# Kernel optimization log

Hardware: AMD Instinct MI355X
Metric: run time of the kernel (lower is better)

## Reference

```python
import jax, jax.numpy as jnp
import numpy as np

B, S, EMBED, HEADS = 2, 2048, 1024, 16
HEAD = EMBED // HEADS


def setup_inputs() -> dict:
    key = jax.random.key(0)
    ks = jax.random.split(key, 8)
    inp = {
        "values": jax.random.normal(ks[0], (B, S, EMBED), jnp.float32),
        "keys": jax.random.normal(ks[1], (B, S, EMBED), jnp.float32),
        "queries": jax.random.normal(ks[2], (B, S, EMBED), jnp.float32),
        # causal mask, broadcast over batch and heads; masked_fill where mask==0
        "mask": jnp.tril(jnp.ones((S, S), jnp.bool_))[None, None, :, :],
        # torch nn.Linear weights: y = x @ W.T (+ b)
        "Wv": jax.random.normal(ks[3], (HEAD, HEAD), jnp.float32) / np.sqrt(HEAD),
        "Wk": jax.random.normal(ks[4], (HEAD, HEAD), jnp.float32) / np.sqrt(HEAD),
        "Wq": jax.random.normal(ks[5], (HEAD, HEAD), jnp.float32) / np.sqrt(HEAD),
        "Wo": jax.random.normal(ks[6], (EMBED, EMBED), jnp.float32) / np.sqrt(EMBED),
        "bo": jax.random.normal(ks[7], (EMBED,), jnp.float32) * 0.01,
    }
    return inp


def reference(values, keys, queries, mask, Wv, Wk, Wq, Wo, bo):
    N, Lq = queries.shape[0], queries.shape[1]
    Lk = keys.shape[1]
    # split heads: [B, L, H, D]
    v = values.reshape(N, -1, HEADS, HEAD) @ Wv.T
    k = keys.reshape(N, Lk, HEADS, HEAD) @ Wk.T
    q = queries.reshape(N, Lq, HEADS, HEAD) @ Wq.T
    # scores [B, H, Lq, Lk]
    energy = jnp.einsum('bqhd,bkhd->bhqk', q, k)
    energy = jnp.where(mask, energy, jnp.float32(-1e20))
    attn = jax.nn.softmax(energy / np.sqrt(HEAD), axis=-1)
    out = jnp.einsum('bhqk,bkhd->bqhd', attn, v).reshape(N, Lq, EMBED)
    return out @ Wo.T + bo
```

## Files before the change

kernel.cpp:

```cpp
#include <hip/hip_runtime.h>
#include <hip/hip_bf16.h>
#include <math.h>

constexpr int Bc = 2;
constexpr int Sc = 2048;
constexpr int E  = 1024;
constexpr int Hn = 16;
constexpr int Dh = 64;

typedef short bf16x8 __attribute__((ext_vector_type(8)));
typedef float f32x4  __attribute__((ext_vector_type(4)));

#define MFMA16(a, b, c) __builtin_amdgcn_mfma_f32_16x16x32_bf16((a), (b), (c), 0, 0, 0)

constexpr float QSCALE = 0.125f * 1.4426950408889634f;
constexpr float FIXED_M2 = 18.0f;

__device__ inline bf16x8 load8(const __hip_bfloat16* p) {
    return *reinterpret_cast<const bf16x8*>(p);
}

__device__ inline unsigned short f2b(float x) {
    __hip_bfloat16 h = __float2bfloat16(x);
    unsigned short u;
    __builtin_memcpy(&u, &h, 2);
    return u;
}

__device__ inline ushort4 pack4(float a, float b, float c, float d) {
    __hip_bfloat162 lo = __float22bfloat162_rn(make_float2(a, b));
    __hip_bfloat162 hi = __float22bfloat162_rn(make_float2(c, d));
    ushort4 u;
    __builtin_memcpy(&u.x, &lo, 4);
    __builtin_memcpy(&u.z, &hi, 4);
    return u;
}

__device__ inline bf16x8 cvt8(const float* p) {
    float4 a = *reinterpret_cast<const float4*>(p);
    float4 b = *reinterpret_cast<const float4*>(p + 4);
    ushort4 lo = pack4(a.x, a.y, a.z, a.w);
    ushort4 hi = pack4(b.x, b.y, b.z, b.w);
    bf16x8 r;
    __builtin_memcpy(&r, &lo, 8);
    __builtin_memcpy(reinterpret_cast<char*>(&r) + 8, &hi, 8);
    return r;
}

__device__ inline float fast_exp2(float x) {
#if __has_builtin(__builtin_amdgcn_exp2f)
    return __builtin_amdgcn_exp2f(x);
#else
    return exp2f(x);
#endif
}


__global__ __launch_bounds__(256) void cvt_w(
    const float* __restrict__ Wo, const float* __restrict__ Wq,
    const float* __restrict__ Wk, const float* __restrict__ Wv,
    __hip_bfloat16* __restrict__ Wf, __hip_bfloat16* __restrict__ Wf3) {
    const int i = blockIdx.x * 256 + threadIdx.x;
    if (i < 131072) {
        const int l16 = i & 15, quad = (i >> 4) & 3;
        const int kk = (i >> 6) & 31, ct = i >> 11;
        bf16x8 v = cvt8(Wo + (size_t)(ct * 16 + l16) * E + kk * 32 + quad * 8);
        *reinterpret_cast<bf16x8*>(Wf + (size_t)i * 8) = v;
    } else {
        const int idx = i - 131072;
        const int m = idx >> 9, r = idx & 511;
        const int lane = r & 63, nh = r >> 6;
        const int nt = nh >> 1, half = nh & 1;
        const int quad = lane >> 4, l16 = lane & 15;
        const float* Wm = (m == 0) ? Wq : (m == 1) ? Wk : Wv;
        bf16x8 v = cvt8(Wm + (nt * 16 + l16) * 64 + half * 32 + quad * 8);
        *reinterpret_cast<bf16x8*>(Wf3 + (size_t)idx * 8) = v;
    }
}

__global__ __launch_bounds__(256) void qkv_proj(
    const float* __restrict__ vals,
    const float* __restrict__ keys,
    const float* __restrict__ quer,
    const __hip_bfloat16* __restrict__ Wf3,
    __hip_bfloat16* __restrict__ Qf,
    __hip_bfloat16* __restrict__ Kf,
    __hip_bfloat16* __restrict__ Vf)
{
    __shared__ __align__(16) __hip_bfloat16 X[3][64 * 72];

    const int bid = blockIdx.x;
    const int st  = bid & 31;
    const int h   = (bid >> 5) & 15;
    const int b   = bid >> 9;
    const int sbase = st * 64;
    const int tid = threadIdx.x;

    const float* srcs[3] = { quer, keys, vals };
#pragma unroll
    for (int m = 0; m < 3; ++m) {
        for (int i = tid; i < 512; i += 256) {
            const int r = i >> 3, c = i & 7;
            bf16x8 v = cvt8(srcs[m] + (size_t)(b * Sc + sbase + r) * E + h * 64 + c * 8);
            *reinterpret_cast<bf16x8*>(&X[m][r * 72 + c * 8]) = v;
        }
    }
    __syncthreads();

    const int lane = tid & 63, w = tid >> 6;
    const int quad = lane >> 4, l16 = lane & 15;
    const int bh = b * Hn + h;
    const size_t bhoff = (size_t)bh * 131072;

#pragma unroll
    for (int m = 0; m < 2; ++m) {
        bf16x8 xb0 = load8(&X[m][(w * 16 + l16) * 72 + quad * 8]);
        bf16x8 xb1 = load8(&X[m][(w * 16 + l16) * 72 + quad * 8 + 32]);
#pragma unroll
        for (int ntd = 0; ntd < 4; ++ntd) {
            bf16x8 wa0 = load8(Wf3 + ((size_t)(m * 8 + ntd * 2 + 0) * 64 + lane) * 8);
            bf16x8 wa1 = load8(Wf3 + ((size_t)(m * 8 + ntd * 2 + 1) * 64 + lane) * 8);
            f32x4 acc = (f32x4){0.f, 0.f, 0.f, 0.f};
            acc = MFMA16(wa0, xb0, acc);
            acc = MFMA16(wa1, xb1, acc);
            const int half   = ntd >> 1;
            const int quad_f = (ntd & 1) * 2 + (quad >> 1);
            const int j0     = (quad & 1) * 4;
            if (m == 0) {
                const int t = st * 4 + w;
                *reinterpret_cast<ushort4*>(
                    Qf + bhoff + ((size_t)(t * 2 + half) * 64 + quad_f * 16 + l16) * 8 + j0) =
                    pack4(acc[0] * QSCALE, acc[1] * QSCALE, acc[2] * QSCALE, acc[3] * QSCALE);
            } else {
                *reinterpret_cast<ushort4*>(
                    Kf + bhoff + (((size_t)(st * 4 + w) * 2 + half) * 64 + quad_f * 16 + l16) * 8 + j0) =
                    pack4(acc[0], acc[1], acc[2], acc[3]);
            }
        }
    }

    {
        bf16x8 xa0 = load8(&X[2][(w * 16 + l16) * 72 + quad * 8]);
        bf16x8 xa1 = load8(&X[2][(w * 16 + l16) * 72 + quad * 8 + 32]);
        const int half   = w >> 1;
        const int quad_f = (w & 1) * 2 + (quad >> 1);
        const int j0     = (quad & 1) * 4;
#pragma unroll
        for (int nt = 0; nt < 4; ++nt) {
            bf16x8 wb0 = load8(Wf3 + ((size_t)(16 + nt * 2 + 0) * 64 + lane) * 8);
            bf16x8 wb1 = load8(Wf3 + ((size_t)(16 + nt * 2 + 1) * 64 + lane) * 8);
            f32x4 acc = (f32x4){0.f, 0.f, 0.f, 0.f};
            acc = MFMA16(xa0, wb0, acc);
            acc = MFMA16(xa1, wb1, acc);
            *reinterpret_cast<ushort4*>(
                Vf + bhoff + (((size_t)(st * 4 + nt) * 2 + half) * 64 + quad_f * 16 + l16) * 8 + j0) =
                pack4(acc[0], acc[1], acc[2], acc[3]);
        }
    }
}

__global__ __launch_bounds__(256) void flash_attn(
    const __hip_bfloat16* __restrict__ Qf,
    const __hip_bfloat16* __restrict__ Kf,
    const __hip_bfloat16* __restrict__ Vf,
    __hip_bfloat16* __restrict__ Af)
{
    __shared__ __align__(16) __hip_bfloat16 P[4][16 * 72];
    __shared__ __align__(16) float OB[4][16 * 68];
    __shared__ float LB[4][16];

    const int bid = blockIdx.x;
    const int bh = bid & 31;
    const int ip = bid >> 5;
    const int h  = bh & 15;
    const int b  = bh >> 4;
    const int tid = threadIdx.x, lane = tid & 63, w = tid >> 6;
    const int quad = lane >> 4, l16 = lane & 15;
    const int p  = w >> 1;
    const int hf = w & 1;
    const int j  = ip * 2 + p;

    const __hip_bfloat16* Qp = Qf + (size_t)bh * 131072;
    const __hip_bfloat16* Kp = Kf + (size_t)bh * 131072;
    const __hip_bfloat16* Vp = Vf + (size_t)bh * 131072;

    bf16x8 onesf;
#pragma unroll
    for (int q = 0; q < 8; ++q) onesf[q] = (short)0x3F80;

#pragma unroll
    for (int side = 0; side < 2; ++side) {
        const int t  = side ? j : (127 - j);
        const int nk = (t >> 2) + 1;
        const int r0 = t * 16;

        const bf16x8 qf0 = load8(Qp + ((size_t)(t * 2 + 0) * 64 + lane) * 8);
        const bf16x8 qf1 = load8(Qp + ((size_t)(t * 2 + 1) * 64 + lane) * 8);

        f32x4 oa[4];
#pragma unroll
        for (int nt = 0; nt < 4; ++nt) oa[nt] = (f32x4){0.f, 0.f, 0.f, 0.f};
        f32x4 lsacc = (f32x4){0.f, 0.f, 0.f, 0.f};

        if (hf < nk) {
            bf16x8 ka[4], kb[4];
#pragma unroll
            for (int nt = 0; nt < 4; ++nt) {
                const size_t o = (((size_t)hf * 4 + nt) * 2) * 64 * 8;
                ka[nt] = load8(Kp + o + lane * 8);
                kb[nt] = load8(Kp + o + 512 + lane * 8);
            }
            for (int kt = hf; kt < nk; kt += 2) {
                bf16x8 va[4], vb[4];
#pragma unroll
                for (int nt = 0; nt < 4; ++nt) {
                    const size_t o = (((size_t)kt * 4 + nt) * 2) * 64 * 8;
                    va[nt] = load8(Vp + o + lane * 8);
                    vb[nt] = load8(Vp + o + 512 + lane * 8);
                }
                const int nkt = (kt + 2 < nk) ? kt + 2 : kt;
                bf16x8 na[4], nb[4];
#pragma unroll
                for (int nt = 0; nt < 4; ++nt) {
                    const size_t o = (((size_t)nkt * 4 + nt) * 2) * 64 * 8;
                    na[nt] = load8(Kp + o + lane * 8);
                    nb[nt] = load8(Kp + o + 512 + lane * 8);
                }
                const int kbase = kt * 64;
                f32x4 sc[4];
#pragma unroll
                for (int ntk = 0; ntk < 4; ++ntk) {
                    f32x4 z = (f32x4){0.f, 0.f, 0.f, 0.f};
                    z = MFMA16(ka[ntk], qf0, z);
                    z = MFMA16(kb[ntk], qf1, z);
                    sc[ntk] = z;
                }
                if (kt == nk - 1) {
                    const int qrow = r0 + l16;
#pragma unroll
                    for (int ntk = 0; ntk < 4; ++ntk) {
#pragma unroll
                        for (int r = 0; r < 4; ++r)
                            if (kbase + ntk * 16 + quad * 4 + r > qrow)
                                sc[ntk][r] = -1e30f;
                    }
                }
#pragma unroll
                for (int ntk = 0; ntk < 4; ++ntk) {
                    const float p0 = fast_exp2(sc[ntk][0] - FIXED_M2);
                    const float p1 = fast_exp2(sc[ntk][1] - FIXED_M2);
                    const float p2 = fast_exp2(sc[ntk][2] - FIXED_M2);
                    const float p3 = fast_exp2(sc[ntk][3] - FIXED_M2);
                    *reinterpret_cast<ushort4*>(
                        &P[w][l16 * 72 + ntk * 16 + quad * 4]) = pack4(p0, p1, p2, p3);
                }
                bf16x8 pf0 = load8(&P[w][l16 * 72 + quad * 8]);
                bf16x8 pf1 = load8(&P[w][l16 * 72 + quad * 8 + 32]);
#pragma unroll
                for (int nt = 0; nt < 4; ++nt) {
                    oa[nt] = MFMA16(va[nt], pf0, oa[nt]);
                    oa[nt] = MFMA16(vb[nt], pf1, oa[nt]);
                }
                lsacc = MFMA16(onesf, pf0, lsacc);
                lsacc = MFMA16(onesf, pf1, lsacc);
#pragma unroll
                for (int nt = 0; nt < 4; ++nt) { ka[nt] = na[nt]; kb[nt] = nb[nt]; }
            }
        }
        const float ls = lsacc[0];

        const int slot = p * 2 + side;
        if (hf == 1) {
#pragma unroll
            for (int nt = 0; nt < 4; ++nt)
                *reinterpret_cast<float4*>(&OB[slot][l16 * 68 + nt * 16 + quad * 4]) =
                    (float4){ oa[nt][0], oa[nt][1], oa[nt][2], oa[nt][3] };
            if (quad == 0) LB[slot][l16] = ls;
        }
        __syncthreads();
        if (hf == 0) {
            const float inv = 1.0f / (ls + LB[slot][l16]);
            const int rt = b * 128 + t;
#pragma unroll
            for (int nt = 0; nt < 4; ++nt) {
                float4 ob = *reinterpret_cast<float4*>(&OB[slot][l16 * 68 + nt * 16 + quad * 4]);
                const int kk     = h * 2 + (nt >> 1);
                const int quad_f = (nt & 1) * 2 + (quad >> 1);
                const int j0     = (quad & 1) * 4;
                *reinterpret_cast<ushort4*>(
                    Af + (((size_t)rt * 32 + kk) * 64 + quad_f * 16 + l16) * 8 + j0) =
                    pack4((oa[nt][0] + ob.x) * inv, (oa[nt][1] + ob.y) * inv,
                          (oa[nt][2] + ob.z) * inv, (oa[nt][3] + ob.w) * inv);
            }
        }
    }
}

__global__ __launch_bounds__(256) void out_proj(
    const __hip_bfloat16* __restrict__ Af,
    const __hip_bfloat16* __restrict__ Wf,
    const float* __restrict__ bo,
    float* __restrict__ out)
{
    const int bid = blockIdx.x;
    const int cb = bid & 15;
    const int rb = bid >> 4;
    const int tid = threadIdx.x, lane = tid & 63, w = tid >> 6;
    const int quad = lane >> 4, l16 = lane & 15;
    const int rt0 = rb * 8 + w;
    const int cbase = cb * 64;

    const __hip_bfloat16* pa0 = Af + ((size_t)rt0 * 32) * 512 + lane * 8;
    const __hip_bfloat16* pa1 = pa0 + 4 * 32 * 512;
    const __hip_bfloat16* pw  = Wf + ((size_t)cb * 4 * 32) * 512 + lane * 8;

    f32x4 acc[2][4];
#pragma unroll
    for (int u = 0; u < 2; ++u)
#pragma unroll
        for (int nt = 0; nt < 4; ++nt) acc[u][nt] = (f32x4){0.f, 0.f, 0.f, 0.f};

    bf16x8 af0[2], af1[2], bf[4][2];
#pragma unroll
    for (int s = 0; s < 2; ++s) {
        const size_t ko = (size_t)s * 512;
        af0[s] = load8(pa0 + ko);
        af1[s] = load8(pa1 + ko);
#pragma unroll
        for (int nt = 0; nt < 4; ++nt) bf[nt][s] = load8(pw + (size_t)nt * 32 * 512 + ko);
    }

    for (int kk = 0; kk < 32; kk += 2) {
#pragma unroll
        for (int s = 0; s < 2; ++s) {
            const int kn = kk + 2 + s;
            const size_t ko = (size_t)((kn < 32) ? kn : kk + s) * 512;
            bf16x8 naf0 = load8(pa0 + ko), naf1 = load8(pa1 + ko);
            bf16x8 nbf[4];
#pragma unroll
            for (int nt = 0; nt < 4; ++nt) nbf[nt] = load8(pw + (size_t)nt * 32 * 512 + ko);
#pragma unroll
            for (int nt = 0; nt < 4; ++nt) {
                acc[0][nt] = MFMA16(af0[s], bf[nt][s], acc[0][nt]);
                acc[1][nt] = MFMA16(af1[s], bf[nt][s], acc[1][nt]);
            }
            af0[s] = naf0; af1[s] = naf1;
#pragma unroll
            for (int nt = 0; nt < 4; ++nt) bf[nt][s] = nbf[nt];
        }
    }
#pragma unroll
    for (int nt = 0; nt < 4; ++nt) {
        const float bv = bo[cbase + nt * 16 + l16];
#pragma unroll
        for (int u = 0; u < 2; ++u)
#pragma unroll
            for (int r = 0; r < 4; ++r) {
                const int row = (rt0 + u * 4) * 16 + quad * 4 + r;
                out[(size_t)row * E + cbase + nt * 16 + l16] = acc[u][nt][r] + bv;
            }
    }
}

extern "C" void kernel_launch(void* const* d_in, const int* in_sizes, int n_in,
                              void* d_out, int out_size, void* d_ws, size_t ws_size,
                              hipStream_t stream) {
    const float* vals = (const float*)d_in[0];
    const float* keys = (const float*)d_in[1];
    const float* quer = (const float*)d_in[2];
    const float* Wv = (const float*)d_in[4];
    const float* Wk = (const float*)d_in[5];
    const float* Wq = (const float*)d_in[6];
    const float* Wo = (const float*)d_in[7];
    const float* bo = (const float*)d_in[8];
    float* out = (float*)d_out;

    __hip_bfloat16* ws = (__hip_bfloat16*)d_ws;
    constexpr size_t NTOK = (size_t)Bc * Hn * Sc * Dh;
    __hip_bfloat16* Qw  = ws;
    __hip_bfloat16* Kw  = ws + NTOK;
    __hip_bfloat16* Vw  = ws + 2 * NTOK;
    __hip_bfloat16* Aw  = ws + 3 * NTOK;
    __hip_bfloat16* Wof = ws + 4 * NTOK;
    __hip_bfloat16* Wf3 = Wof + (size_t)E * E;

    hipLaunchKernelGGL(cvt_w, dim3(518), dim3(256), 0, stream, Wo, Wq, Wk, Wv, Wof, Wf3);
    hipLaunchKernelGGL(qkv_proj, dim3(Bc * Hn * (Sc / 64)), dim3(256), 0, stream,
                       vals, keys, quer, Wf3, Qw, Kw, Vw);
    hipLaunchKernelGGL(flash_attn, dim3(32 * 32), dim3(256), 0, stream,
                       Qw, Kw, Vw, Aw);
    hipLaunchKernelGGL(out_proj, dim3(32 * 16), dim3(256), 0, stream,
                       Aw, Wof, bo, out);
}
```

Measured before the change: 176.6 us.

## Process two adjacent query tiles per wave sharing K/V loads, longest blocks first

Flash attention blocks now use two waves that each handle a pair of adjacent 16-row query tiles, so every K and V fragment loaded is reused for two query tiles. The old front/back pairing of query tiles for load balance is replaced by a grid of 128-thread blocks ordered so the heaviest (longest causal) blocks launch first. The fixed softmax offset is folded into the MFMA accumulator init, and K prefetching across iterations is dropped. This cuts global K/V traffic per query row but raises register pressure and removes software prefetch.

```diff
diff --git a/kernel.cpp b/kernel.cpp
--- a/kernel.cpp
+++ b/kernel.cpp
@@ -159,26 +159,25 @@
     }
 }
 
-__global__ __launch_bounds__(256) void flash_attn(
+__global__ __launch_bounds__(128, 4) void flash_attn(
     const __hip_bfloat16* __restrict__ Qf,
     const __hip_bfloat16* __restrict__ Kf,
     const __hip_bfloat16* __restrict__ Vf,
     __hip_bfloat16* __restrict__ Af)
 {
-    __shared__ __align__(16) __hip_bfloat16 P[4][16 * 72];
-    __shared__ __align__(16) float OB[4][16 * 68];
-    __shared__ float LB[4][16];
+    __shared__ __align__(16) __hip_bfloat16 P[2][2][16 * 72];
+    __shared__ __align__(16) float OB[2][16 * 68];
+    __shared__ float LB[2][16];
 
     const int bid = blockIdx.x;
     const int bh = bid & 31;
-    const int ip = bid >> 5;
+    const int u  = 63 - (bid >> 5);
     const int h  = bh & 15;
     const int b  = bh >> 4;
-    const int tid = threadIdx.x, lane = tid & 63, w = tid >> 6;
+    const int tid = threadIdx.x, lane = tid & 63, hf = tid >> 6;
     const int quad = lane >> 4, l16 = lane & 15;
-    const int p  = w >> 1;
-    const int hf = w & 1;
-    const int j  = ip * 2 + p;
+    const int t0 = 2 * u, t1 = 2 * u + 1;
+    const int nk = (u >> 1) + 1;
 
     const __hip_bfloat16* Qp = Qf + (size_t)bh * 131072;
     const __hip_bfloat16* Kp = Kf + (size_t)bh * 131072;
@@ -188,109 +187,137 @@
 #pragma unroll
     for (int q = 0; q < 8; ++q) onesf[q] = (short)0x3F80;
 
-#pragma unroll
-    for (int side = 0; side < 2; ++side) {
-        const int t  = side ? j : (127 - j);
-        const int nk = (t >> 2) + 1;
-        const int r0 = t * 16;
-
-        const bf16x8 qf0 = load8(Qp + ((size_t)(t * 2 + 0) * 64 + lane) * 8);
-        const bf16x8 qf1 = load8(Qp + ((size_t)(t * 2 + 1) * 64 + lane) * 8);
-
-        f32x4 oa[4];
-#pragma unroll
-        for (int nt = 0; nt < 4; ++nt) oa[nt] = (f32x4){0.f, 0.f, 0.f, 0.f};
-        f32x4 lsacc = (f32x4){0.f, 0.f, 0.f, 0.f};
-
-        if (hf < nk) {
-            bf16x8 ka[4], kb[4];
+    const bf16x8 q0a = load8(Qp + ((size_t)(t0 * 2 + 0) * 64 + lane) * 8);
+    const bf16x8 q0b = load8(Qp + ((size_t)(t0 * 2 + 1) * 64 + lane) * 8);
+    const bf16x8 q1a = load8(Qp + ((size_t)(t1 * 2 + 0) * 64 + lane) * 8);
+    const bf16x8 q1b = load8(Qp + ((size_t)(t1 * 2 + 1) * 64 + lane) * 8);
+
+    f32x4 oa0[4], oa1[4];
+#pragma unroll
+    for (int nt = 0; nt < 4; ++nt) {
+        oa0[nt] = (f32x4){0.f, 0.f, 0.f, 0.f};
+        oa1[nt] = (f32x4){0.f, 0.f, 0.f, 0.f};
+    }
+    f32x4 ls0 = (f32x4){0.f, 0.f, 0.f, 0.f};
+    f32x4 ls1 = (f32x4){0.f, 0.f, 0.f, 0.f};
+
+    for (int kt = hf; kt < nk; kt += 2) {
+        bf16x8 ka[4], kb[4];
+#pragma unroll
+        for (int nt = 0; nt < 4; ++nt) {
+            const size_t o = (((size_t)kt * 4 + nt) * 2) * 512;
+            ka[nt] = load8(Kp + o + lane * 8);
+            kb[nt] = load8(Kp + o + 512 + lane * 8);
+        }
+        const int kbase = kt * 64;
+        const bool diag = (kt == nk - 1);
+
+        f32x4 sc[4];
+#pragma unroll
+        for (int ntk = 0; ntk < 4; ++ntk) {
+            f32x4 z = (f32x4){-FIXED_M2, -FIXED_M2, -FIXED_M2, -FIXED_M2};
+            z = MFMA16(ka[ntk], q0a, z);
+            z = MFMA16(kb[ntk], q0b, z);
+            sc[ntk] = z;
+        }
+        if (diag) {
+            const int qrow = t0 * 16 + l16;
+#pragma unroll
+            for (int ntk = 0; ntk < 4; ++ntk)
+#pragma unroll
+                for (int r = 0; r < 4; ++r)
+                    if (kbase + ntk * 16 + quad * 4 + r > qrow) sc[ntk][r] = -1e30f;
+        }
+#pragma unroll
+        for (int ntk = 0; ntk < 4; ++ntk) {
+            *reinterpret_cast<ushort4*>(&P[hf][0][l16 * 72 + ntk * 16 + quad * 4]) =
+                pack4(fast_exp2(sc[ntk][0]), fast_exp2(sc[ntk][1]),
+                      fast_exp2(sc[ntk][2]), fast_exp2(sc[ntk][3]));
+        }
+
+#pragma unroll
+        for (int ntk = 0; ntk < 4; ++ntk) {
+            f32x4 z = (f32x4){-FIXED_M2, -FIXED_M2, -FIXED_M2, -FIXED_M2};
+            z = MFMA16(ka[ntk], q1a, z);
+            z = MFMA16(kb[ntk], q1b, z);
+            sc[ntk] = z;
+        }
+        if (diag) {
+            const int qrow = t1 * 16 + l16;
+#pragma unroll
+            for (int ntk = 0; ntk < 4; ++ntk)
+#pragma unroll
+                for (int r = 0; r < 4; ++r)
+                    if (kbase + ntk * 16 + quad * 4 + r > qrow) sc[ntk][r] = -1e30f;
+        }
+
+        bf16x8 va[4], vb[4];
+#pragma unroll
+        for (int nt = 0; nt < 4; ++nt) {
+            const size_t o = (((size_t)kt * 4 + nt) * 2) * 512;
+            va[nt] = load8(Vp + o + lane * 8);
+            vb[nt] = load8(Vp + o + 512 + lane * 8);
+        }
+
+#pragma unroll
+        for (int ntk = 0; ntk < 4; ++ntk) {
+            *reinterpret_cast<ushort4*>(&P[hf][1][l16 * 72 + ntk * 16 + quad * 4]) =
+                pack4(fast_exp2(sc[ntk][0]), fast_exp2(sc[ntk][1]),
+                      fast_exp2(sc[ntk][2]), fast_exp2(sc[ntk][3]));
+        }
+
+        {
+            bf16x8 pf0 = load8(&P[hf][0][l16 * 72 + quad * 8]);
+            bf16x8 pf1 = load8(&P[hf][0][l16 * 72 + quad * 8 + 32]);
 #pragma unroll
             for (int nt = 0; nt < 4; ++nt) {
-                const size_t o = (((size_t)hf * 4 + nt) * 2) * 64 * 8;
-                ka[nt] = load8(Kp + o + lane * 8);
-                kb[nt] = load8(Kp + o + 512 + lane * 8);
-            }
-            for (int kt = hf; kt < nk; kt += 2) {
-                bf16x8 va[4], vb[4];
-#pragma unroll
-                for (int nt = 0; nt < 4; ++nt) {
-                    const size_t o = (((size_t)kt * 4 + nt) * 2) * 64 * 8;
-                    va[nt] = load8(Vp + o + lane * 8);
-                    vb[nt] = load8(Vp + o + 512 + lane * 8);
-                }
-                const int nkt = (kt + 2 < nk) ? kt + 2 : kt;
-                bf16x8 na[4], nb[4];
-#pragma unroll
-                for (int nt = 0; nt < 4; ++nt) {
-                    const size_t o = (((size_t)nkt * 4 + nt) * 2) * 64 * 8;
-                    na[nt] = load8(Kp + o + lane * 8);
-                    nb[nt] = load8(Kp + o + 512 + lane * 8);
-                }
-                const int kbase = kt * 64;
-                f32x4 sc[4];
-#pragma unroll
-                for (int ntk = 0; ntk < 4; ++ntk) {
-                    f32x4 z = (f32x4){0.f, 0.f, 0.f, 0.f};
-                    z = MFMA16(ka[ntk], qf0, z);
-                    z = MFMA16(kb[ntk], qf1, z);
-                    sc[ntk] = z;
-                }
-                if (kt == nk - 1) {
-                    const int qrow = r0 + l16;
-#pragma unroll
-                    for (int ntk = 0; ntk < 4; ++ntk) {
-#pragma unroll
-                        for (int r = 0; r < 4; ++r)
-                            if (kbase + ntk * 16 + quad * 4 + r > qrow)
-                                sc[ntk][r] = -1e30f;
-                    }
-                }
-#pragma unroll
-                for (int ntk = 0; ntk < 4; ++ntk) {
-                    const float p0 = fast_exp2(sc[ntk][0] - FIXED_M2);
-                    const float p1 = fast_exp2(sc[ntk][1] - FIXED_M2);
-                    const float p2 = fast_exp2(sc[ntk][2] - FIXED_M2);
-                    const float p3 = fast_exp2(sc[ntk][3] - FIXED_M2);
-                    *reinterpret_cast<ushort4*>(
-                        &P[w][l16 * 72 + ntk * 16 + quad * 4]) = pack4(p0, p1, p2, p3);
-                }
-                bf16x8 pf0 = load8(&P[w][l16 * 72 + quad * 8]);
-                bf16x8 pf1 = load8(&P[w][l16 * 72 + quad * 8 + 32]);
-#pragma unroll
-                for (int nt = 0; nt < 4; ++nt) {
-                    oa[nt] = MFMA16(va[nt], pf0, oa[nt]);
-                    oa[nt] = MFMA16(vb[nt], pf1, oa[nt]);
-                }
-                lsacc = MFMA16(onesf, pf0, lsacc);
-                lsacc = MFMA16(onesf, pf1, lsacc);
-#pragma unroll
-                for (int nt = 0; nt < 4; ++nt) { ka[nt] = na[nt]; kb[nt] = nb[nt]; }
-            }
-        }
-        const float ls = lsacc[0];
-
-        const int slot = p * 2 + side;
-        if (hf == 1) {
-#pragma unroll
-            for (int nt = 0; nt < 4; ++nt)
-                *reinterpret_cast<float4*>(&OB[slot][l16 * 68 + nt * 16 + quad * 4]) =
-                    (float4){ oa[nt][0], oa[nt][1], oa[nt][2], oa[nt][3] };
-            if (quad == 0) LB[slot][l16] = ls;
-        }
-        __syncthreads();
-        if (hf == 0) {
-            const float inv = 1.0f / (ls + LB[slot][l16]);
-            const int rt = b * 128 + t;
+                oa0[nt] = MFMA16(va[nt], pf0, oa0[nt]);
+                oa0[nt] = MFMA16(vb[nt], pf1, oa0[nt]);
+            }
+            ls0 = MFMA16(onesf, pf0, ls0);
+            ls0 = MFMA16(onesf, pf1, ls0);
+        }
+        {
+            bf16x8 pf0 = load8(&P[hf][1][l16 * 72 + quad * 8]);
+            bf16x8 pf1 = load8(&P[hf][1][l16 * 72 + quad * 8 + 32]);
 #pragma unroll
             for (int nt = 0; nt < 4; ++nt) {
-                float4 ob = *reinterpret_cast<float4*>(&OB[slot][l16 * 68 + nt * 16 + quad * 4]);
+                oa1[nt] = MFMA16(va[nt], pf0, oa1[nt]);
+                oa1[nt] = MFMA16(vb[nt], pf1, oa1[nt]);
+            }
+            ls1 = MFMA16(onesf, pf0, ls1);
+            ls1 = MFMA16(onesf, pf1, ls1);
+        }
+    }
+
+    if (hf == 1) {
+#pragma unroll
+        for (int nt = 0; nt < 4; ++nt) {
+            *reinterpret_cast<float4*>(&OB[0][l16 * 68 + nt * 16 + quad * 4]) =
+                (float4){ oa0[nt][0], oa0[nt][1], oa0[nt][2], oa0[nt][3] };
+            *reinterpret_cast<float4*>(&OB[1][l16 * 68 + nt * 16 + quad * 4]) =
+                (float4){ oa1[nt][0], oa1[nt][1], oa1[nt][2], oa1[nt][3] };
+        }
+        if (quad == 0) { LB[0][l16] = ls0[0]; LB[1][l16] = ls1[0]; }
+    }
+    __syncthreads();
+    if (hf == 0) {
+#pragma unroll
+        for (int tl = 0; tl < 2; ++tl) {
+            const float lsw = (tl == 0) ? ls0[0] : ls1[0];
+            const float inv = 1.0f / (lsw + LB[tl][l16]);
+            const int rt = b * 128 + (tl == 0 ? t0 : t1);
+#pragma unroll
+            for (int nt = 0; nt < 4; ++nt) {
+                float4 ob = *reinterpret_cast<float4*>(&OB[tl][l16 * 68 + nt * 16 + quad * 4]);
+                const f32x4 ov = (tl == 0) ? oa0[nt] : oa1[nt];
                 const int kk     = h * 2 + (nt >> 1);
                 const int quad_f = (nt & 1) * 2 + (quad >> 1);
                 const int j0     = (quad & 1) * 4;
                 *reinterpret_cast<ushort4*>(
                     Af + (((size_t)rt * 32 + kk) * 64 + quad_f * 16 + l16) * 8 + j0) =
-                    pack4((oa[nt][0] + ob.x) * inv, (oa[nt][1] + ob.y) * inv,
-                          (oa[nt][2] + ob.z) * inv, (oa[nt][3] + ob.w) * inv);
+                    pack4((ov[0] + ob.x) * inv, (ov[1] + ob.y) * inv,
+                          (ov[2] + ob.z) * inv, (ov[3] + ob.w) * inv);
             }
         }
     }
@@ -387,7 +414,7 @@
     hipLaunchKernelGGL(cvt_w, dim3(518), dim3(256), 0, stream, Wo, Wq, Wk, Wv, Wof, Wf3);
     hipLaunchKernelGGL(qkv_proj, dim3(Bc * Hn * (Sc / 64)), dim3(256), 0, stream,
                        vals, keys, quer, Wf3, Qw, Kw, Vw);
-    hipLaunchKernelGGL(flash_attn, dim3(32 * 32), dim3(256), 0, stream,
+    hipLaunchKernelGGL(flash_attn, dim3(64 * 32), dim3(128), 0, stream,
                        Qw, Kw, Vw, Aw);
     hipLaunchKernelGGL(out_proj, dim3(32 * 16), dim3(256), 0, stream,
                        Aw, Wof, bo, out);
```

After: 173.3 us. About the same (-1.9%).

## Restructure flash attention so each wave processes four query tiles per K/V block

Applied to the files above, without the earlier changes.

The attention kernel now launches 128-thread blocks. Each of the two waves handles four consecutive 16-row query tiles against its half of the key tiles, so every loaded K/V fragment is reused across four query tiles instead of one. The old pairing of short and long causal tiles, which balanced work within a block, is replaced by a reversed block order so the longest blocks start first. Score and PV MFMAs for pairs of tiles are interleaved through double-buffered LDS P slots, and the fixed max offset is folded into the accumulator init. In exchange, register pressure rises (16 output accumulators per lane) and per-block work becomes uneven.

```diff
diff --git a/kernel.cpp b/kernel.cpp
--- a/kernel.cpp
+++ b/kernel.cpp
@@ -159,26 +159,24 @@
     }
 }
 
-__global__ __launch_bounds__(256) void flash_attn(
+__global__ __launch_bounds__(128, 2) void flash_attn(
     const __hip_bfloat16* __restrict__ Qf,
     const __hip_bfloat16* __restrict__ Kf,
     const __hip_bfloat16* __restrict__ Vf,
     __hip_bfloat16* __restrict__ Af)
 {
-    __shared__ __align__(16) __hip_bfloat16 P[4][16 * 72];
+    __shared__ __align__(16) __hip_bfloat16 P[2][2][16 * 72];
     __shared__ __align__(16) float OB[4][16 * 68];
     __shared__ float LB[4][16];
 
     const int bid = blockIdx.x;
     const int bh = bid & 31;
-    const int ip = bid >> 5;
+    const int u  = 31 - (bid >> 5);
     const int h  = bh & 15;
     const int b  = bh >> 4;
-    const int tid = threadIdx.x, lane = tid & 63, w = tid >> 6;
+    const int tid = threadIdx.x, lane = tid & 63, hf = tid >> 6;
     const int quad = lane >> 4, l16 = lane & 15;
-    const int p  = w >> 1;
-    const int hf = w & 1;
-    const int j  = ip * 2 + p;
+    const int nk = u + 1;
 
     const __hip_bfloat16* Qp = Qf + (size_t)bh * 131072;
     const __hip_bfloat16* Kp = Kf + (size_t)bh * 131072;
@@ -188,109 +186,126 @@
 #pragma unroll
     for (int q = 0; q < 8; ++q) onesf[q] = (short)0x3F80;
 
-#pragma unroll
-    for (int side = 0; side < 2; ++side) {
-        const int t  = side ? j : (127 - j);
-        const int nk = (t >> 2) + 1;
-        const int r0 = t * 16;
-
-        const bf16x8 qf0 = load8(Qp + ((size_t)(t * 2 + 0) * 64 + lane) * 8);
-        const bf16x8 qf1 = load8(Qp + ((size_t)(t * 2 + 1) * 64 + lane) * 8);
-
-        f32x4 oa[4];
-#pragma unroll
-        for (int nt = 0; nt < 4; ++nt) oa[nt] = (f32x4){0.f, 0.f, 0.f, 0.f};
-        f32x4 lsacc = (f32x4){0.f, 0.f, 0.f, 0.f};
-
-        if (hf < nk) {
-            bf16x8 ka[4], kb[4];
+    bf16x8 qa[4], qb[4];
+#pragma unroll
+    for (int i = 0; i < 4; ++i) {
+        qa[i] = load8(Qp + ((size_t)((4 * u + i) * 2 + 0) * 64 + lane) * 8);
+        qb[i] = load8(Qp + ((size_t)((4 * u + i) * 2 + 1) * 64 + lane) * 8);
+    }
+
+    f32x4 oa[4][4];
+    f32x4 ls[4];
+#pragma unroll
+    for (int i = 0; i < 4; ++i) {
+        ls[i] = (f32x4){0.f, 0.f, 0.f, 0.f};
+#pragma unroll
+        for (int nt = 0; nt < 4; ++nt) oa[i][nt] = (f32x4){0.f, 0.f, 0.f, 0.f};
+    }
+
+    bf16x8 ka[4], kb[4];
+#pragma unroll
+    for (int nt = 0; nt < 4; ++nt) {
+        const size_t o = (((size_t)hf * 4 + nt) * 2) * 512;
+        ka[nt] = load8(Kp + o + lane * 8);
+        kb[nt] = load8(Kp + o + 512 + lane * 8);
+    }
+
+    bf16x8 va[4], vb[4];
+
+    for (int kt = hf; kt < nk; kt += 2) {
+#pragma unroll
+        for (int nt = 0; nt < 4; ++nt) {
+            const size_t o = (((size_t)kt * 4 + nt) * 2) * 512;
+            va[nt] = load8(Vp + o + lane * 8);
+            vb[nt] = load8(Vp + o + 512 + lane * 8);
+        }
+
+        const int kbase = kt * 64;
+        const bool diag = (kt == nk - 1);
+
+        auto scores = [&](int i, int s) {
+            f32x4 sc[4];
+#pragma unroll
+            for (int ntk = 0; ntk < 4; ++ntk) {
+                f32x4 z = (f32x4){-FIXED_M2, -FIXED_M2, -FIXED_M2, -FIXED_M2};
+                z = MFMA16(ka[ntk], qa[i], z);
+                z = MFMA16(kb[ntk], qb[i], z);
+                sc[ntk] = z;
+            }
+            if (diag) {
+                const int qrow = (4 * u + i) * 16 + l16;
+#pragma unroll
+                for (int ntk = 0; ntk < 4; ++ntk)
+#pragma unroll
+                    for (int r = 0; r < 4; ++r)
+                        if (kbase + ntk * 16 + quad * 4 + r > qrow) sc[ntk][r] = -1e30f;
+            }
+#pragma unroll
+            for (int ntk = 0; ntk < 4; ++ntk) {
+                *reinterpret_cast<ushort4*>(&P[hf][s][l16 * 72 + ntk * 16 + quad * 4]) =
+                    pack4(fast_exp2(sc[ntk][0]), fast_exp2(sc[ntk][1]),
+                          fast_exp2(sc[ntk][2]), fast_exp2(sc[ntk][3]));
+            }
+        };
+        auto pv = [&](int i, int s) {
+            bf16x8 pf0 = load8(&P[hf][s][l16 * 72 + quad * 8]);
+            bf16x8 pf1 = load8(&P[hf][s][l16 * 72 + quad * 8 + 32]);
 #pragma unroll
             for (int nt = 0; nt < 4; ++nt) {
-                const size_t o = (((size_t)hf * 4 + nt) * 2) * 64 * 8;
+                oa[i][nt] = MFMA16(va[nt], pf0, oa[i][nt]);
+                oa[i][nt] = MFMA16(vb[nt], pf1, oa[i][nt]);
+            }
+            ls[i] = MFMA16(onesf, pf0, ls[i]);
+            ls[i] = MFMA16(onesf, pf1, ls[i]);
+        };
+
+        scores(0, 0);
+        scores(1, 1);
+        pv(0, 0);
+        pv(1, 1);
+        scores(2, 0);
+        scores(3, 1);
+
+        {
+            const int nkt = (kt + 2 < nk) ? kt + 2 : kt;
+#pragma unroll
+            for (int nt = 0; nt < 4; ++nt) {
+                const size_t o = (((size_t)nkt * 4 + nt) * 2) * 512;
                 ka[nt] = load8(Kp + o + lane * 8);
                 kb[nt] = load8(Kp + o + 512 + lane * 8);
             }
-            for (int kt = hf; kt < nk; kt += 2) {
-                bf16x8 va[4], vb[4];
-#pragma unroll
-                for (int nt = 0; nt < 4; ++nt) {
-                    const size_t o = (((size_t)kt * 4 + nt) * 2) * 64 * 8;
-                    va[nt] = load8(Vp + o + lane * 8);
-                    vb[nt] = load8(Vp + o + 512 + lane * 8);
-                }
-                const int nkt = (kt + 2 < nk) ? kt + 2 : kt;
-                bf16x8 na[4], nb[4];
-#pragma unroll
-                for (int nt = 0; nt < 4; ++nt) {
-                    const size_t o = (((size_t)nkt * 4 + nt) * 2) * 64 * 8;
-                    na[nt] = load8(Kp + o + lane * 8);
-                    nb[nt] = load8(Kp + o + 512 + lane * 8);
-                }
-                const int kbase = kt * 64;
-                f32x4 sc[4];
-#pragma unroll
-                for (int ntk = 0; ntk < 4; ++ntk) {
-                    f32x4 z = (f32x4){0.f, 0.f, 0.f, 0.f};
-                    z = MFMA16(ka[ntk], qf0, z);
-                    z = MFMA16(kb[ntk], qf1, z);
-                    sc[ntk] = z;
-                }
-                if (kt == nk - 1) {
-                    const int qrow = r0 + l16;
-#pragma unroll
-                    for (int ntk = 0; ntk < 4; ++ntk) {
-#pragma unroll
-                        for (int r = 0; r < 4; ++r)
-                            if (kbase + ntk * 16 + quad * 4 + r > qrow)
-                                sc[ntk][r] = -1e30f;
-                    }
-                }
-#pragma unroll
-                for (int ntk = 0; ntk < 4; ++ntk) {
-                    const float p0 = fast_exp2(sc[ntk][0] - FIXED_M2);
-                    const float p1 = fast_exp2(sc[ntk][1] - FIXED_M2);
-                    const float p2 = fast_exp2(sc[ntk][2] - FIXED_M2);
-                    const float p3 = fast_exp2(sc[ntk][3] - FIXED_M2);
-                    *reinterpret_cast<ushort4*>(
-                        &P[w][l16 * 72 + ntk * 16 + quad * 4]) = pack4(p0, p1, p2, p3);
-                }
-                bf16x8 pf0 = load8(&P[w][l16 * 72 + quad * 8]);
-                bf16x8 pf1 = load8(&P[w][l16 * 72 + quad * 8 + 32]);
-#pragma unroll
-                for (int nt = 0; nt < 4; ++nt) {
-                    oa[nt] = MFMA16(va[nt], pf0, oa[nt]);
-                    oa[nt] = MFMA16(vb[nt], pf1, oa[nt]);
-                }
-                lsacc = MFMA16(onesf, pf0, lsacc);
-                lsacc = MFMA16(onesf, pf1, lsacc);
-#pragma unroll
-                for (int nt = 0; nt < 4; ++nt) { ka[nt] = na[nt]; kb[nt] = nb[nt]; }
-            }
-        }
-        const float ls = lsacc[0];
-
-        const int slot = p * 2 + side;
-        if (hf == 1) {
+        }
+
+        pv(2, 0);
+        pv(3, 1);
+    }
+
+    if (hf == 1) {
+#pragma unroll
+        for (int i = 0; i < 4; ++i) {
 #pragma unroll
             for (int nt = 0; nt < 4; ++nt)
-                *reinterpret_cast<float4*>(&OB[slot][l16 * 68 + nt * 16 + quad * 4]) =
-                    (float4){ oa[nt][0], oa[nt][1], oa[nt][2], oa[nt][3] };
-            if (quad == 0) LB[slot][l16] = ls;
-        }
-        __syncthreads();
-        if (hf == 0) {
-            const float inv = 1.0f / (ls + LB[slot][l16]);
-            const int rt = b * 128 + t;
+                *reinterpret_cast<float4*>(&OB[i][l16 * 68 + nt * 16 + quad * 4]) =
+                    (float4){ oa[i][nt][0], oa[i][nt][1], oa[i][nt][2], oa[i][nt][3] };
+            if (quad == 0) LB[i][l16] = ls[i][0];
+        }
+    }
+    __syncthreads();
+    if (hf == 0) {
+#pragma unroll
+        for (int i = 0; i < 4; ++i) {
+            const float inv = 1.0f / (ls[i][0] + LB[i][l16]);
+            const int rt = b * 128 + 4 * u + i;
 #pragma unroll
             for (int nt = 0; nt < 4; ++nt) {
-                float4 ob = *reinterpret_cast<float4*>(&OB[slot][l16 * 68 + nt * 16 + quad * 4]);
+                float4 ob = *reinterpret_cast<float4*>(&OB[i][l16 * 68 + nt * 16 + quad * 4]);
                 const int kk     = h * 2 + (nt >> 1);
                 const int quad_f = (nt & 1) * 2 + (quad >> 1);
                 const int j0     = (quad & 1) * 4;
                 *reinterpret_cast<ushort4*>(
                     Af + (((size_t)rt * 32 + kk) * 64 + quad_f * 16 + l16) * 8 + j0) =
-                    pack4((oa[nt][0] + ob.x) * inv, (oa[nt][1] + ob.y) * inv,
-                          (oa[nt][2] + ob.z) * inv, (oa[nt][3] + ob.w) * inv);
+                    pack4((oa[i][nt][0] + ob.x) * inv, (oa[i][nt][1] + ob.y) * inv,
+                          (oa[i][nt][2] + ob.z) * inv, (oa[i][nt][3] + ob.w) * inv);
             }
         }
     }
@@ -387,7 +402,7 @@
     hipLaunchKernelGGL(cvt_w, dim3(518), dim3(256), 0, stream, Wo, Wq, Wk, Wv, Wof, Wf3);
     hipLaunchKernelGGL(qkv_proj, dim3(Bc * Hn * (Sc / 64)), dim3(256), 0, stream,
                        vals, keys, quer, Wf3, Qw, Kw, Vw);
-    hipLaunchKernelGGL(flash_attn, dim3(32 * 32), dim3(256), 0, stream,
+    hipLaunchKernelGGL(flash_attn, dim3(32 * 32), dim3(128), 0, stream,
                        Qw, Kw, Vw, Aw);
     hipLaunchKernelGGL(out_proj, dim3(32 * 16), dim3(256), 0, stream,
                        Aw, Wof, bo, out);
```

New measurement: 171.4 us. 3.0% less time.
